# Kernel tuning notes

Hardware: AMD Instinct MI355X
Metric: run time of the kernel (lower is better)

Reference implementation:

```python
import jax, jax.numpy as jnp
import numpy as np

B, N, C = 256, 25, 256          # batch, joints, in_features
H = 256                          # hidden_features (MLP hidden = H // 2 = 128)


def _build_chain_paths(n):
    """Flatten shortest paths of a chain skeleton (parent[i]=i-1) into
    (heads, ends, pair_ids): edge k of path i->j contributes
    src[:, ends[e]] - src[:, heads[e]] accumulated into pair i*n+j."""
    heads, ends, pair = [], [], []
    for i in range(n):
        for j in range(n):
            step = 1 if j >= i else -1
            cur = i
            while cur != j:
                heads.append(cur)
                ends.append(cur + step)
                pair.append(i * n + j)
                cur += step
    return (np.asarray(heads, np.int32), np.asarray(ends, np.int32),
            np.asarray(pair, np.int32))


def setup_inputs() -> dict:
    key = jax.random.key(0)
    k_src, k_w1, k_w2 = jax.random.split(key, 3)
    heads, ends, pair_ids = _build_chain_paths(N)  # E = 5200 for N=25
    src = jax.random.normal(k_src, (B, N, C), dtype=jnp.float32)
    # torch Linear weights: [out, in], no bias for both edgefeat linears
    W1 = jax.random.normal(k_w1, (H // 2, C), dtype=jnp.float32) / np.sqrt(C)
    W2 = jax.random.normal(k_w2, (1, H // 2), dtype=jnp.float32) / np.sqrt(H // 2)
    alpha = jnp.full((1,), 0.25, dtype=jnp.float32)  # PReLU init
    return {"src": src, "heads": jnp.asarray(heads), "ends": jnp.asarray(ends),
            "pair_ids": jnp.asarray(pair_ids), "W1": W1, "alpha": alpha, "W2": W2}


def reference(src, heads, ends, pair_ids, W1, alpha, W2):
    b, n, c = src.shape
    # gather-subtract along every path edge: [B, E, C]
    diff = src[:, ends, :] - src[:, heads, :]
    # accumulate per (i, j) pair: segment_sum over leading axis -> [N*N, B, C]
    acc = jax.ops.segment_sum(jnp.transpose(diff, (1, 0, 2)), pair_ids,
                              num_segments=n * n)
    edge_feat = jnp.transpose(acc.reshape(n, n, b, c), (2, 0, 1, 3))  # [B,N,N,C]
    h = jnp.einsum('bijc,hc->bijh', edge_feat, W1)   # [B,N,N,H//2]
    h = jnp.where(h >= 0, h, alpha * h)              # PReLU (single shared alpha)
    return jnp.einsum('bijh,oh->bijo', h, W2)        # [B,N,N,1]
```

## Files before the change

kernel.cpp:

```cpp
#include <hip/hip_runtime.h>

#define NJ   25
#define CIN  256
#define HH   128
#define SS   264
#define US   136

typedef _Float16 h2  __attribute__((ext_vector_type(2)));
typedef _Float16 h4  __attribute__((ext_vector_type(4)));
typedef _Float16 h8f __attribute__((ext_vector_type(8)));
typedef __attribute__((ext_vector_type(4))) float f32x4;

__device__ __forceinline__ unsigned short f2h_bits(float f) {
    union { _Float16 h; unsigned short u; } v; v.h = (_Float16)f; return v.u;
}
__device__ __forceinline__ unsigned pack2h(float a, float b) {
    return (unsigned)f2h_bits(a) | ((unsigned)f2h_bits(b) << 16);
}
__device__ __forceinline__ h2 as_h2(unsigned u) {
    union { unsigned u; h2 h; } v; v.u = u; return v.h;
}

__global__ __launch_bounds__(256) void prep_w(
    const float* __restrict__ W1, const float* __restrict__ W2,
    unsigned short* __restrict__ w1frag, unsigned* __restrict__ w2pk)
{
    const int gid = blockIdx.x * 256 + threadIdx.x;
    if (gid < 4096) {
        const int lane = gid & 63, kt = (gid >> 6) & 7, nt = gid >> 9;
        const int row = nt * 16 + (lane & 15);
        const int k0  = kt * 32 + (lane >> 4) * 8;
        const float* base = W1 + (size_t)row * CIN + k0;
        float4 x = *(const float4*)base;
        float4 y = *(const float4*)(base + 4);
        uint4 o;
        o.x = pack2h(x.x, x.y); o.y = pack2h(x.z, x.w);
        o.z = pack2h(y.x, y.y); o.w = pack2h(y.z, y.w);
        *(uint4*)(w1frag + (size_t)gid * 8) = o;
    } else if (gid < 4096 + HH / 2) {
        const int id = gid - 4096;
        w2pk[id] = pack2h(W2[2 * id], W2[2 * id + 1]);
    }
}

__global__ __launch_bounds__(512) void fused_edge_mlp_v8(
    const float* __restrict__ src,
    const unsigned short* __restrict__ w1frag,
    const unsigned* __restrict__ w2pk,
    const float* __restrict__ Aarr,
    float* __restrict__ out)
{
    __shared__ unsigned short s_lds[NJ * SS];
    __shared__ unsigned short u16[NJ * US];
    __shared__ float s_s[NJ];

    const int b    = blockIdx.x;
    const int t    = threadIdx.x;
    const int w    = t >> 6;
    const int lane = t & 63;
    const int ln15 = lane & 15;
    const int quad = lane >> 4;
    const int hcol = w * 16 + ln15;

    {
        const float4* s4 = (const float4*)(src + (size_t)b * NJ * CIN);
        for (int idx = t; idx < NJ * CIN / 4; idx += 512) {
            const int n = idx >> 6, k4 = idx & 63;
            float4 v = s4[idx];
            uint2 o = make_uint2(pack2h(v.x, v.y), pack2h(v.z, v.w));
            *(uint2*)&s_lds[n * SS + k4 * 4] = o;
        }
    }
    __syncthreads();

    {
        const h8f* w1p = (const h8f*)w1frag + (w * 8) * 64 + lane;
        h8f bfrag[8];
        #pragma unroll
        for (int kt = 0; kt < 8; ++kt) bfrag[kt] = w1p[kt * 64];

        const int r1   = 16 + ln15;
        const bool r1ok = (r1 < NJ);
        const int cbase = quad * 8;

        f32x4 acc0 = {0.f, 0.f, 0.f, 0.f};
        f32x4 acc1 = {0.f, 0.f, 0.f, 0.f};
        #pragma unroll
        for (int kt = 0; kt < 8; ++kt) {
            const int co = kt * 32 + cbase;
            h4 lo0 = *(const h4*)&s_lds[ln15 * SS + co];
            h4 hi0 = *(const h4*)&s_lds[ln15 * SS + co + 4];
            h8f a0;
            a0[0] = lo0[0]; a0[1] = lo0[1]; a0[2] = lo0[2]; a0[3] = lo0[3];
            a0[4] = hi0[0]; a0[5] = hi0[1]; a0[6] = hi0[2]; a0[7] = hi0[3];
            h8f a1 = {};
            if (r1ok) {
                h4 lo1 = *(const h4*)&s_lds[r1 * SS + co];
                h4 hi1 = *(const h4*)&s_lds[r1 * SS + co + 4];
                a1[0] = lo1[0]; a1[1] = lo1[1]; a1[2] = lo1[2]; a1[3] = lo1[3];
                a1[4] = hi1[0]; a1[5] = hi1[1]; a1[6] = hi1[2]; a1[7] = hi1[3];
            }
            acc0 = __builtin_amdgcn_mfma_f32_16x16x32_f16(a0, bfrag[kt], acc0, 0, 0, 0);
            acc1 = __builtin_amdgcn_mfma_f32_16x16x32_f16(a1, bfrag[kt], acc1, 0, 0, 0);
        }

        #pragma unroll
        for (int r = 0; r < 4; ++r) {
            int m0 = quad * 4 + r;
            if (m0 < NJ) u16[m0 * US + hcol] = f2h_bits(acc0[r]);
            int m1 = 16 + quad * 4 + r;
            if (m1 < NJ) u16[m1 * US + hcol] = f2h_bits(acc1[r]);
        }
    }
    __syncthreads();

    const float alpha = Aarr[0];
    float* outb = out + (size_t)b * (NJ * NJ);
    const uint4* w2v = (const uint4*)w2pk;

    float M = 0.f;
    int i = 0, j = 0;
    if (t < 300) {
        i = (int)((49.0f - sqrtf(2401.0f - 8.0f * (float)t)) * 0.5f);
        {
            int Si = (49 * i - i * i) >> 1;
            if (t < Si) { --i; }
            else { int Sn = (49 * (i + 1) - (i + 1) * (i + 1)) >> 1; if (t >= Sn) ++i; }
        }
        const int S = (49 * i - i * i) >> 1;
        j = t - S + i + 1;

        const uint4* ujp = (const uint4*)(u16 + j * US);
        const uint4* uip = (const uint4*)(u16 + i * US);
        #pragma unroll
        for (int h8 = 0; h8 < 16; ++h8) {
            uint4 a = ujp[h8], c = uip[h8], ww = w2v[h8];
            h2 mx;
            mx = __builtin_elementwise_max(as_h2(a.x), as_h2(c.x));
            M  = __builtin_amdgcn_fdot2(mx, as_h2(ww.x), M, false);
            mx = __builtin_elementwise_max(as_h2(a.y), as_h2(c.y));
            M  = __builtin_amdgcn_fdot2(mx, as_h2(ww.y), M, false);
            mx = __builtin_elementwise_max(as_h2(a.z), as_h2(c.z));
            M  = __builtin_amdgcn_fdot2(mx, as_h2(ww.z), M, false);
            mx = __builtin_elementwise_max(as_h2(a.w), as_h2(c.w));
            M  = __builtin_amdgcn_fdot2(mx, as_h2(ww.w), M, false);
        }
    } else if (t < 300 + NJ) {
        const int r = t - 300;
        const uint4* up = (const uint4*)(u16 + r * US);
        float s = 0.f;
        #pragma unroll
        for (int h8 = 0; h8 < 16; ++h8) {
            uint4 a = up[h8], ww = w2v[h8];
            s = __builtin_amdgcn_fdot2(as_h2(a.x), as_h2(ww.x), s, false);
            s = __builtin_amdgcn_fdot2(as_h2(a.y), as_h2(ww.y), s, false);
            s = __builtin_amdgcn_fdot2(as_h2(a.z), as_h2(ww.z), s, false);
            s = __builtin_amdgcn_fdot2(as_h2(a.w), as_h2(ww.w), s, false);
        }
        s_s[r] = s;
    }
    __syncthreads();

    if (t < 300) {
        const float sj = s_s[j], si = s_s[i];
        const float Mw = (1.f - alpha) * M;
        outb[i * NJ + j] = Mw + alpha * sj - si;
        outb[j * NJ + i] = Mw + alpha * si - sj;
    } else if (t >= 325 && t < 350) {
        const int r = t - 325;
        outb[r * (NJ + 1)] = 0.f;
    }
}

extern "C" void kernel_launch(void* const* d_in, const int* in_sizes, int n_in,
                              void* d_out, int out_size, void* d_ws, size_t ws_size,
                              hipStream_t stream) {
    const float* src   = (const float*)d_in[0];
    const float* W1    = (const float*)d_in[4];
    const float* alpha = (const float*)d_in[5];
    const float* W2    = (const float*)d_in[6];
    float* out = (float*)d_out;

    const int B = in_sizes[0] / (NJ * CIN);
    unsigned short* w1frag = (unsigned short*)d_ws;
    unsigned*       w2pk   = (unsigned*)(w1frag + 4096 * 8);

    prep_w<<<17, 256, 0, stream>>>(W1, W2, w1frag, w2pk);
    fused_edge_mlp_v8<<<B, 512, 0, stream>>>(src, w1frag, w2pk, alpha, out);
}
```

Baseline: 72.49 us.

## Fold weight prep into main kernel, staging W1 and W2 through LDS

```diff
diff --git a/kernel.cpp b/kernel.cpp
--- a/kernel.cpp
+++ b/kernel.cpp
@@ -7,7 +7,6 @@
 #define US   136
 
 typedef _Float16 h2  __attribute__((ext_vector_type(2)));
-typedef _Float16 h4  __attribute__((ext_vector_type(4)));
 typedef _Float16 h8f __attribute__((ext_vector_type(8)));
 typedef __attribute__((ext_vector_type(4))) float f32x4;
 
@@ -21,37 +20,17 @@
     union { unsigned u; h2 h; } v; v.u = u; return v.h;
 }
 
-__global__ __launch_bounds__(256) void prep_w(
-    const float* __restrict__ W1, const float* __restrict__ W2,
-    unsigned short* __restrict__ w1frag, unsigned* __restrict__ w2pk)
-{
-    const int gid = blockIdx.x * 256 + threadIdx.x;
-    if (gid < 4096) {
-        const int lane = gid & 63, kt = (gid >> 6) & 7, nt = gid >> 9;
-        const int row = nt * 16 + (lane & 15);
-        const int k0  = kt * 32 + (lane >> 4) * 8;
-        const float* base = W1 + (size_t)row * CIN + k0;
-        float4 x = *(const float4*)base;
-        float4 y = *(const float4*)(base + 4);
-        uint4 o;
-        o.x = pack2h(x.x, x.y); o.y = pack2h(x.z, x.w);
-        o.z = pack2h(y.x, y.y); o.w = pack2h(y.z, y.w);
-        *(uint4*)(w1frag + (size_t)gid * 8) = o;
-    } else if (gid < 4096 + HH / 2) {
-        const int id = gid - 4096;
-        w2pk[id] = pack2h(W2[2 * id], W2[2 * id + 1]);
-    }
-}
-
-__global__ __launch_bounds__(512) void fused_edge_mlp_v8(
+__global__ __launch_bounds__(512) void fused_edge_mlp_v9(
     const float* __restrict__ src,
-    const unsigned short* __restrict__ w1frag,
-    const unsigned* __restrict__ w2pk,
+    const float* __restrict__ W1,
     const float* __restrict__ Aarr,
+    const float* __restrict__ W2,
     float* __restrict__ out)
 {
+    __shared__ unsigned short w1_lds[HH * SS];
     __shared__ unsigned short s_lds[NJ * SS];
     __shared__ unsigned short u16[NJ * US];
+    __shared__ unsigned w2s[HH / 2];
     __shared__ float s_s[NJ];
 
     const int b    = blockIdx.x;
@@ -63,23 +42,27 @@
     const int hcol = w * 16 + ln15;
 
     {
+        const float4* w4 = (const float4*)W1;
+        #pragma unroll 4
+        for (int idx = t; idx < HH * CIN / 4; idx += 512) {
+            const int r = idx >> 6, k4 = idx & 63;
+            float4 v = w4[idx];
+            *(uint2*)&w1_lds[r * SS + k4 * 4] =
+                make_uint2(pack2h(v.x, v.y), pack2h(v.z, v.w));
+        }
         const float4* s4 = (const float4*)(src + (size_t)b * NJ * CIN);
         for (int idx = t; idx < NJ * CIN / 4; idx += 512) {
             const int n = idx >> 6, k4 = idx & 63;
             float4 v = s4[idx];
-            uint2 o = make_uint2(pack2h(v.x, v.y), pack2h(v.z, v.w));
-            *(uint2*)&s_lds[n * SS + k4 * 4] = o;
+            *(uint2*)&s_lds[n * SS + k4 * 4] =
+                make_uint2(pack2h(v.x, v.y), pack2h(v.z, v.w));
         }
+        if (t < HH / 2) w2s[t] = pack2h(W2[2 * t], W2[2 * t + 1]);
     }
     __syncthreads();
 
     {
-        const h8f* w1p = (const h8f*)w1frag + (w * 8) * 64 + lane;
-        h8f bfrag[8];
-        #pragma unroll
-        for (int kt = 0; kt < 8; ++kt) bfrag[kt] = w1p[kt * 64];
-
-        const int r1   = 16 + ln15;
+        const int r1    = 16 + ln15;
         const bool r1ok = (r1 < NJ);
         const int cbase = quad * 8;
 
@@ -88,20 +71,12 @@
         #pragma unroll
         for (int kt = 0; kt < 8; ++kt) {
             const int co = kt * 32 + cbase;
-            h4 lo0 = *(const h4*)&s_lds[ln15 * SS + co];
-            h4 hi0 = *(const h4*)&s_lds[ln15 * SS + co + 4];
-            h8f a0;
-            a0[0] = lo0[0]; a0[1] = lo0[1]; a0[2] = lo0[2]; a0[3] = lo0[3];
-            a0[4] = hi0[0]; a0[5] = hi0[1]; a0[6] = hi0[2]; a0[7] = hi0[3];
+            h8f bf = *(const h8f*)&w1_lds[hcol * SS + co];
+            h8f a0 = *(const h8f*)&s_lds[ln15 * SS + co];
             h8f a1 = {};
-            if (r1ok) {
-                h4 lo1 = *(const h4*)&s_lds[r1 * SS + co];
-                h4 hi1 = *(const h4*)&s_lds[r1 * SS + co + 4];
-                a1[0] = lo1[0]; a1[1] = lo1[1]; a1[2] = lo1[2]; a1[3] = lo1[3];
-                a1[4] = hi1[0]; a1[5] = hi1[1]; a1[6] = hi1[2]; a1[7] = hi1[3];
-            }
-            acc0 = __builtin_amdgcn_mfma_f32_16x16x32_f16(a0, bfrag[kt], acc0, 0, 0, 0);
-            acc1 = __builtin_amdgcn_mfma_f32_16x16x32_f16(a1, bfrag[kt], acc1, 0, 0, 0);
+            if (r1ok) a1 = *(const h8f*)&s_lds[r1 * SS + co];
+            acc0 = __builtin_amdgcn_mfma_f32_16x16x32_f16(a0, bf, acc0, 0, 0, 0);
+            acc1 = __builtin_amdgcn_mfma_f32_16x16x32_f16(a1, bf, acc1, 0, 0, 0);
         }
 
         #pragma unroll
@@ -116,7 +91,7 @@
 
     const float alpha = Aarr[0];
     float* outb = out + (size_t)b * (NJ * NJ);
-    const uint4* w2v = (const uint4*)w2pk;
+    const uint4* w2v = (const uint4*)w2s;
 
     float M = 0.f;
     int i = 0, j = 0;
@@ -182,9 +157,5 @@
     float* out = (float*)d_out;
 
     const int B = in_sizes[0] / (NJ * CIN);
-    unsigned short* w1frag = (unsigned short*)d_ws;
-    unsigned*       w2pk   = (unsigned*)(w1frag + 4096 * 8);
-
-    prep_w<<<17, 256, 0, stream>>>(W1, W2, w1frag, w2pk);
-    fused_edge_mlp_v8<<<B, 512, 0, stream>>>(src, w1frag, w2pk, alpha, out);
+    fused_edge_mlp_v9<<<B, 512, 0, stream>>>(src, W1, alpha, W2, out);
 }
```

New measurement: 72.12 us. No clear change (-0.5%).
